# Kernel tuning notes

Hardware: AMD Instinct MI355X
Metric: run time of the kernel (lower is better)

The kernel has to match this reference:

```python
import jax, jax.numpy as jnp
import numpy as np

IN_CH = 128
HID = 256   # 2 * out_channels
OUT_CH = 128
N_NODES = 10000
N_EDGES = 640000


def setup_inputs() -> dict:
    key = jax.random.key(0)
    ks = jax.random.split(key, 6)
    x = jax.random.normal(ks[0], (N_NODES, IN_CH), dtype=jnp.float32)
    edge_index = jax.random.randint(ks[1], (2, N_EDGES), 0, N_NODES, dtype=jnp.int64)
    # GCNConv params (glorot-like scale)
    W1 = jax.random.normal(ks[2], (IN_CH, HID), dtype=jnp.float32) / np.sqrt(IN_CH)
    b1 = jnp.zeros((HID,), dtype=jnp.float32)
    W2 = jax.random.normal(ks[3], (HID, OUT_CH), dtype=jnp.float32) / np.sqrt(HID)
    b2 = jnp.zeros((OUT_CH,), dtype=jnp.float32)
    return {"x": x, "edge_index": edge_index, "W1": W1, "b1": b1, "W2": W2, "b2": b2}


def _gcn_norm(edge_index, n_nodes):
    """Add self-loops and compute symmetric GCN normalization per edge."""
    loops = jnp.arange(n_nodes, dtype=edge_index.dtype)
    src = jnp.concatenate([edge_index[0], loops])  # [E+N]
    dst = jnp.concatenate([edge_index[1], loops])
    deg = jax.ops.segment_sum(jnp.ones_like(dst, dtype=jnp.float32), dst,
                              num_segments=n_nodes)
    dinv = jnp.where(deg > 0, jax.lax.rsqrt(deg), 0.0)
    norm = dinv[src] * dinv[dst]  # [E+N]
    return src, dst, norm


def _gcn_layer(x, W, b, src, dst, norm, n_nodes):
    h = x @ W                                  # [N, F_out]
    msg = h[src] * norm[:, None]               # gather + scale, [E+N, F_out]
    agg = jax.ops.segment_sum(msg, dst, num_segments=n_nodes)
    return agg + b


def reference(x, edge_index, W1, b1, W2, b2):
    n = x.shape[0]
    src, dst, norm = _gcn_norm(edge_index, n)
    h = jax.nn.relu(_gcn_layer(x, W1, b1, src, dst, norm, n))
    out = jax.nn.relu(_gcn_layer(h, W2, b2, src, dst, norm, n))
    return out
```

## Files before the change

### kernel.cpp

```cpp
#include <hip/hip_runtime.h>

#define N_FEAT 128
#define HID 256
#define OUT_CH 128

#define NB 256
#define MAXN 10240
#define CH 16
#define CB (NB / CH)

__device__ __forceinline__ unsigned bf16rn(float f) {
    unsigned u = __float_as_uint(f);
    return (u + 0x7fffu + ((u >> 16) & 1u)) >> 16;
}
__device__ __forceinline__ unsigned pack_bf16x2(float lo, float hi) {
    return bf16rn(lo) | (bf16rn(hi) << 16);
}
__device__ __forceinline__ float2 unpack_bf16x2(unsigned u) {
    float2 r;
    r.x = __uint_as_float(u << 16);
    r.y = __uint_as_float(u & 0xffff0000u);
    return r;
}


__global__ __launch_bounds__(256)
void hist_kernel(const int* __restrict__ dst, unsigned short* __restrict__ bh,
                 int E, int N, int chunk) {
    __shared__ int hist[MAXN];
    for (int i = threadIdx.x; i < N; i += 256) hist[i] = 0;
    __syncthreads();
    int base = blockIdx.x * chunk;
    int lim = min(chunk, E - base);
    for (int i = threadIdx.x; i < lim; i += 256) {
        int d = dst[base + i];
        if (d >= 0 && d < N) atomicAdd(&hist[d], 1);
    }
    __syncthreads();
    unsigned short* out = bh + (size_t)blockIdx.x * N;
    for (int i = threadIdx.x; i < N; i += 256) out[i] = (unsigned short)hist[i];
}

__global__ __launch_bounds__(256)
void colsum_kernel(const unsigned short* __restrict__ bh,
                   int* __restrict__ ps, int N) {
    int j = blockIdx.x * 256 + threadIdx.x;
    if (j >= N) return;
    int c = blockIdx.y;
    int s = 0;
    #pragma unroll
    for (int b = c * CB; b < (c + 1) * CB; b++) s += bh[(size_t)b * N + j];
    ps[(size_t)c * N + j] = s;
}

__global__ __launch_bounds__(256)
void colscan_kernel(int* __restrict__ ps, int* __restrict__ counts, int N) {
    int j = blockIdx.x * 256 + threadIdx.x;
    if (j >= N) return;
    int run = 0;
    #pragma unroll
    for (int c = 0; c < CH; c++) {
        size_t idx = (size_t)c * N + j;
        int t = ps[idx];
        ps[idx] = run;
        run += t;
    }
    counts[j] = run;
}

#define SCAN_T 1024
#define SCAN_MAX_PER 16
__global__ __launch_bounds__(SCAN_T)
void scan_dinv_kernel(const int* __restrict__ counts,
                      int* __restrict__ row_start,
                      float* __restrict__ dinv, int n) {
    int tid = threadIdx.x;
    int per = (n + SCAN_T - 1) / SCAN_T;
    int base = tid * per;
    int local[SCAN_MAX_PER];
    int sum = 0;
    for (int j = 0; j < per; j++) {
        int i = base + j;
        int c = (i < n) ? counts[i] : 0;
        local[j] = sum;
        sum += c;
        if (i < n) dinv[i] = rsqrtf((float)(c + 1));
    }
    int lane = tid & 63;
    int wave = tid >> 6;
    int incl = sum;
    #pragma unroll
    for (int off = 1; off < 64; off <<= 1) {
        int t = __shfl_up(incl, off, 64);
        if (lane >= off) incl += t;
    }
    __shared__ int wsum[16];
    __shared__ int woff[16];
    if (lane == 63) wsum[wave] = incl;
    __syncthreads();
    if (wave == 0) {
        int w = (lane < 16) ? wsum[lane] : 0;
        int v = w;
        #pragma unroll
        for (int off = 1; off < 16; off <<= 1) {
            int t = __shfl_up(v, off, 64);
            if (lane >= off) v += t;
        }
        if (lane < 16) woff[lane] = v - w;
    }
    __syncthreads();
    int thread_excl = woff[wave] + (incl - sum);
    for (int j = 0; j < per; j++) {
        int i = base + j;
        if (i < n) row_start[i] = thread_excl + local[j];
    }
    if (tid == SCAN_T - 1) row_start[n] = thread_excl + sum;
}

__global__ __launch_bounds__(256)
void chunkbase_kernel(unsigned short* __restrict__ bh,
                      const int* __restrict__ ps, int N) {
    int j = blockIdx.x * 256 + threadIdx.x;
    if (j >= N) return;
    int c = blockIdx.y;
    int run = ps[(size_t)c * N + j];
    #pragma unroll
    for (int b = c * CB; b < (c + 1) * CB; b++) {
        size_t idx = (size_t)b * N + j;
        int t = bh[idx];
        bh[idx] = (unsigned short)run;
        run += t;
    }
}

__global__ __launch_bounds__(256)
void scat_kernel(const int* __restrict__ src, const int* __restrict__ dst,
                 const unsigned short* __restrict__ bh,
                 const int* __restrict__ row_start,
                 int* __restrict__ csr_src, int E, int N, int chunk) {
    __shared__ int cur[MAXN];
    const unsigned short* basep = bh + (size_t)blockIdx.x * N;
    for (int i = threadIdx.x; i < N; i += 256)
        cur[i] = row_start[i] + (int)basep[i];
    __syncthreads();
    int base = blockIdx.x * chunk;
    int lim = min(chunk, E - base);
    for (int i = threadIdx.x; i < lim; i += 256) {
        int e = base + i;
        int d = dst[e];
        if (d < 0 || d >= N) continue;
        int pos = atomicAdd(&cur[d], 1);
        if ((unsigned)pos < (unsigned)E) csr_src[pos] = src[e];
    }
}

__global__ void prescale_kernel(const float* __restrict__ x,
                                const float* __restrict__ dinv,
                                unsigned* __restrict__ xs_b, int total4) {
    int i = blockIdx.x * blockDim.x + threadIdx.x;
    if (i < total4) {
        int row = i >> 5;
        float d = dinv[row];
        float4 v = ((const float4*)x)[i];
        uint2 p;
        p.x = pack_bf16x2(v.x * d, v.y * d);
        p.y = pack_bf16x2(v.z * d, v.w * d);
        ((uint2*)xs_b)[i] = p;
    }
}

template <bool EPILOGUE>
__global__ __launch_bounds__(256)
void agg_kernel(const unsigned* __restrict__ featb,
                const float* __restrict__ dinv,
                const int* __restrict__ row_start,
                const int* __restrict__ csr_src,
                const float* __restrict__ bias,
                float* __restrict__ out, int N) {
    int wave = threadIdx.x >> 6;
    int n = blockIdx.x * 4 + wave;
    if (n >= N) return;
    int f = threadIdx.x & 63;
    float dn = dinv[n];
    float2 v = unpack_bf16x2(featb[(size_t)n * 64 + f]);
    float accx = v.x;
    float accy = v.y;
    int e0 = row_start[n];
    int e1 = row_start[n + 1];
    int e = e0;
    for (; e + 16 <= e1; e += 16) {
        int s[16];
        #pragma unroll
        for (int j = 0; j < 16; j++) s[j] = csr_src[e + j];
        unsigned w[16];
        #pragma unroll
        for (int j = 0; j < 16; j++) w[j] = featb[(size_t)s[j] * 64 + f];
        #pragma unroll
        for (int j = 0; j < 16; j++) {
            float2 u = unpack_bf16x2(w[j]);
            accx += u.x;
            accy += u.y;
        }
    }
    for (; e + 4 <= e1; e += 4) {
        int s0 = csr_src[e], s1 = csr_src[e + 1];
        int s2 = csr_src[e + 2], s3 = csr_src[e + 3];
        unsigned w0 = featb[(size_t)s0 * 64 + f];
        unsigned w1 = featb[(size_t)s1 * 64 + f];
        unsigned w2 = featb[(size_t)s2 * 64 + f];
        unsigned w3 = featb[(size_t)s3 * 64 + f];
        float2 u0 = unpack_bf16x2(w0), u1 = unpack_bf16x2(w1);
        float2 u2 = unpack_bf16x2(w2), u3 = unpack_bf16x2(w3);
        accx += u0.x + u1.x + u2.x + u3.x;
        accy += u0.y + u1.y + u2.y + u3.y;
    }
    for (; e < e1; ++e) {
        float2 u = unpack_bf16x2(featb[(size_t)csr_src[e] * 64 + f]);
        accx += u.x;
        accy += u.y;
    }
    accx *= dn;
    accy *= dn;
    if (EPILOGUE) {
        float2 b = ((const float2*)bias)[f];
        accx = fmaxf(accx + b.x, 0.0f);
        accy = fmaxf(accy + b.y, 0.0f);
    }
    float2 r;
    r.x = accx;
    r.y = accy;
    ((float2*)out)[(size_t)n * 64 + f] = r;
}

template <bool BIAS_RELU, bool RSCALE, bool BF16_OUT>
__global__ __launch_bounds__(256)
void gemm_kernel(const float* __restrict__ A,
                 const float* __restrict__ B,
                 const float* __restrict__ bias,
                 const float* __restrict__ rscale,
                 void* __restrict__ Cv, int M, int N, int K) {
    __shared__ float As[16][65];
    __shared__ float Bs[16][64];
    int tid = threadIdx.x;
    int n0 = blockIdx.x * 64;
    int m0 = blockIdx.y * 64;
    int tx = tid & 15;
    int ty = tid >> 4;
    float acc[4][4] = {};
    for (int k0 = 0; k0 < K; k0 += 16) {
        #pragma unroll
        for (int i = 0; i < 4; i++) {
            int lin = tid + 256 * i;
            int m = lin >> 4;
            int k = lin & 15;
            float v = 0.0f;
            if (m0 + m < M) v = A[(size_t)(m0 + m) * K + k0 + k];
            As[k][m] = v;
        }
        #pragma unroll
        for (int i = 0; i < 4; i++) {
            int lin = tid + 256 * i;
            int k = lin >> 6;
            int n = lin & 63;
            Bs[k][n] = B[(size_t)(k0 + k) * N + n0 + n];
        }
        __syncthreads();
        #pragma unroll
        for (int k = 0; k < 16; k++) {
            float ra[4], rb[4];
            #pragma unroll
            for (int i = 0; i < 4; i++) ra[i] = As[k][ty * 4 + i];
            #pragma unroll
            for (int j = 0; j < 4; j++) rb[j] = Bs[k][tx * 4 + j];
            #pragma unroll
            for (int i = 0; i < 4; i++)
                #pragma unroll
                for (int j = 0; j < 4; j++)
                    acc[i][j] = fmaf(ra[i], rb[j], acc[i][j]);
        }
        __syncthreads();
    }
    #pragma unroll
    for (int i = 0; i < 4; i++) {
        int m = m0 + ty * 4 + i;
        if (m >= M) continue;
        float rs = RSCALE ? rscale[m] : 1.0f;
        float v[4];
        #pragma unroll
        for (int j = 0; j < 4; j++) {
            v[j] = acc[i][j];
            if (RSCALE) v[j] *= rs;
            if (BIAS_RELU) v[j] = fmaxf(v[j] + bias[n0 + tx * 4 + j], 0.0f);
        }
        if (BF16_OUT) {
            unsigned* Cb = (unsigned*)Cv;
            size_t base = (size_t)m * (N >> 1) + ((n0 + tx * 4) >> 1);
            Cb[base] = pack_bf16x2(v[0], v[1]);
            Cb[base + 1] = pack_bf16x2(v[2], v[3]);
        } else {
            float* C = (float*)Cv;
            #pragma unroll
            for (int j = 0; j < 4; j++)
                C[(size_t)m * N + n0 + tx * 4 + j] = v[j];
        }
    }
}


static inline size_t align512(size_t x) { return (x + 511) & ~(size_t)511; }

extern "C" void kernel_launch(void* const* d_in, const int* in_sizes, int n_in,
                              void* d_out, int out_size, void* d_ws, size_t ws_size,
                              hipStream_t stream) {
    const float* x = (const float*)d_in[0];
    const int* ei = (const int*)d_in[1];
    const float* W1 = (const float*)d_in[2];
    const float* b1 = (const float*)d_in[3];
    const float* W2 = (const float*)d_in[4];
    const float* b2 = (const float*)d_in[5];
    float* out = (float*)d_out;

    const int N = in_sizes[0] / N_FEAT;
    const int E = in_sizes[1] / 2;
    const int* src = ei;
    const int* dst = ei + E;

    char* ws = (char*)d_ws;
    size_t off = 0;
    float* dinv = (float*)(ws + off);    off += align512((size_t)N * 4);
    int* counts = (int*)(ws + off);      off += align512((size_t)N * 4);
    int* row_start = (int*)(ws + off);   off += align512((size_t)(N + 1) * 4);
    int* csr_src = (int*)(ws + off);     off += align512((size_t)E * 4);
    unsigned* xs_b = (unsigned*)(ws + off); off += align512((size_t)N * 64 * 4);
    float* h = (float*)(ws + off);       off += align512((size_t)N * HID * 4);
    unsigned* t_b = (unsigned*)(ws + off); off += align512((size_t)N * 64 * 4);
    int* ps = (int*)(ws + off);          off += align512((size_t)CH * N * 4);
    unsigned short* bh = (unsigned short*)(ws + off);
    off += align512((size_t)NB * N * 2);
    (void)ws_size;
    float* agg1 = out;
    const int chunk = (E + NB - 1) / NB;
    const int NJ = (N + 255) / 256;

    hist_kernel<<<NB, 256, 0, stream>>>(dst, bh, E, N, chunk);
    colsum_kernel<<<dim3(NJ, CH), 256, 0, stream>>>(bh, ps, N);
    colscan_kernel<<<NJ, 256, 0, stream>>>(ps, counts, N);
    scan_dinv_kernel<<<1, SCAN_T, 0, stream>>>(counts, row_start, dinv, N);
    chunkbase_kernel<<<dim3(NJ, CH), 256, 0, stream>>>(bh, ps, N);
    scat_kernel<<<NB, 256, 0, stream>>>(src, dst, bh, row_start, csr_src, E, N, chunk);

    {
        int total4 = N * N_FEAT / 4;
        prescale_kernel<<<(total4 + 255) / 256, 256, 0, stream>>>(x, dinv, xs_b, total4);
    }

    agg_kernel<false><<<(N + 3) / 4, 256, 0, stream>>>(xs_b, dinv, row_start, csr_src,
                                                       nullptr, agg1, N);

    {
        dim3 grid(HID / 64, (N + 63) / 64);
        gemm_kernel<true, false, false><<<grid, 256, 0, stream>>>(
            agg1, W1, b1, nullptr, h, N, HID, N_FEAT);
    }

    {
        dim3 grid(OUT_CH / 64, (N + 63) / 64);
        gemm_kernel<false, true, true><<<grid, 256, 0, stream>>>(
            h, W2, nullptr, dinv, t_b, N, OUT_CH, HID);
    }

    agg_kernel<true><<<(N + 3) / 4, 256, 0, stream>>>(t_b, dinv, row_start, csr_src,
                                                      b2, out, N);
}
```

Baseline: 194.9 us.

## Split wave across two edges per step in aggregation, vectorize GEMM tile loads

The aggregation kernel now has each half-wave handle alternate edges, loading 8 bytes per lane and reading neighbour indices as int2 pairs. The two halves are combined with a cross-half shuffle. This gives wider gather transactions and more edges in flight per wave, at the cost of odd-start and odd-tail handling and idle lanes in those edge cases. The GEMM now stages A and B with float4 global loads and reads LDS as float4. The dinv computation moves from the single-block scan into the parallel colscan kernel, which shortens the serial scan.

After: 248.4 us. +27.4%, slower.

```diff
diff --git a/kernel.cpp b/kernel.cpp
--- a/kernel.cpp
+++ b/kernel.cpp
@@ -54,7 +54,8 @@
 }
 
 __global__ __launch_bounds__(256)
-void colscan_kernel(int* __restrict__ ps, int* __restrict__ counts, int N) {
+void colscan_kernel(int* __restrict__ ps, int* __restrict__ counts,
+                    float* __restrict__ dinv, int N) {
     int j = blockIdx.x * 256 + threadIdx.x;
     if (j >= N) return;
     int run = 0;
@@ -66,14 +67,14 @@
         run += t;
     }
     counts[j] = run;
+    dinv[j] = rsqrtf((float)(run + 1));
 }
 
 #define SCAN_T 1024
 #define SCAN_MAX_PER 16
 __global__ __launch_bounds__(SCAN_T)
-void scan_dinv_kernel(const int* __restrict__ counts,
-                      int* __restrict__ row_start,
-                      float* __restrict__ dinv, int n) {
+void scan_kernel(const int* __restrict__ counts,
+                 int* __restrict__ row_start, int n) {
     int tid = threadIdx.x;
     int per = (n + SCAN_T - 1) / SCAN_T;
     int base = tid * per;
@@ -84,7 +85,6 @@
         int c = (i < n) ? counts[i] : 0;
         local[j] = sum;
         sum += c;
-        if (i < n) dinv[i] = rsqrtf((float)(c + 1));
     }
     int lane = tid & 63;
     int wave = tid >> 6;
@@ -180,56 +180,73 @@
     int wave = threadIdx.x >> 6;
     int n = blockIdx.x * 4 + wave;
     if (n >= N) return;
-    int f = threadIdx.x & 63;
+    int l = threadIdx.x & 63;
+    int half = l >> 5;
+    int fl = l & 31;
+    const uint2* feat2 = (const uint2*)featb;
+    float a0 = 0.f, a1 = 0.f, a2 = 0.f, a3 = 0.f;
+    if (half == 0) {
+        uint2 s = feat2[(size_t)n * 32 + fl];
+        float2 u0 = unpack_bf16x2(s.x), u1 = unpack_bf16x2(s.y);
+        a0 = u0.x; a1 = u0.y; a2 = u1.x; a3 = u1.y;
+    }
+    int e0 = row_start[n], e1 = row_start[n + 1];
+    int e = e0;
+    if ((e & 1) && e < e1) {
+        if (half == 0) {
+            uint2 w = feat2[(size_t)csr_src[e] * 32 + fl];
+            float2 u0 = unpack_bf16x2(w.x), u1 = unpack_bf16x2(w.y);
+            a0 += u0.x; a1 += u0.y; a2 += u1.x; a3 += u1.y;
+        }
+        e++;
+    }
+    const int2* cs2 = (const int2*)csr_src;
+    for (; e + 32 <= e1; e += 32) {
+        int2 p[16];
+        #pragma unroll
+        for (int j = 0; j < 16; j++) p[j] = cs2[(e >> 1) + j];
+        uint2 w[16];
+        #pragma unroll
+        for (int j = 0; j < 16; j++) {
+            int s = half ? p[j].y : p[j].x;
+            w[j] = feat2[(size_t)s * 32 + fl];
+        }
+        #pragma unroll
+        for (int j = 0; j < 16; j++) {
+            float2 u0 = unpack_bf16x2(w[j].x), u1 = unpack_bf16x2(w[j].y);
+            a0 += u0.x; a1 += u0.y; a2 += u1.x; a3 += u1.y;
+        }
+    }
+    for (; e + 2 <= e1; e += 2) {
+        int2 p = cs2[e >> 1];
+        int s = half ? p.y : p.x;
+        uint2 w = feat2[(size_t)s * 32 + fl];
+        float2 u0 = unpack_bf16x2(w.x), u1 = unpack_bf16x2(w.y);
+        a0 += u0.x; a1 += u0.y; a2 += u1.x; a3 += u1.y;
+    }
+    if (e < e1 && half == 0) {
+        uint2 w = feat2[(size_t)csr_src[e] * 32 + fl];
+        float2 u0 = unpack_bf16x2(w.x), u1 = unpack_bf16x2(w.y);
+        a0 += u0.x; a1 += u0.y; a2 += u1.x; a3 += u1.y;
+    }
+    a0 += __shfl_xor(a0, 32, 64);
+    a1 += __shfl_xor(a1, 32, 64);
+    a2 += __shfl_xor(a2, 32, 64);
+    a3 += __shfl_xor(a3, 32, 64);
     float dn = dinv[n];
-    float2 v = unpack_bf16x2(featb[(size_t)n * 64 + f]);
-    float accx = v.x;
-    float accy = v.y;
-    int e0 = row_start[n];
-    int e1 = row_start[n + 1];
-    int e = e0;
-    for (; e + 16 <= e1; e += 16) {
-        int s[16];
-        #pragma unroll
-        for (int j = 0; j < 16; j++) s[j] = csr_src[e + j];
-        unsigned w[16];
-        #pragma unroll
-        for (int j = 0; j < 16; j++) w[j] = featb[(size_t)s[j] * 64 + f];
-        #pragma unroll
-        for (int j = 0; j < 16; j++) {
-            float2 u = unpack_bf16x2(w[j]);
-            accx += u.x;
-            accy += u.y;
-        }
-    }
-    for (; e + 4 <= e1; e += 4) {
-        int s0 = csr_src[e], s1 = csr_src[e + 1];
-        int s2 = csr_src[e + 2], s3 = csr_src[e + 3];
-        unsigned w0 = featb[(size_t)s0 * 64 + f];
-        unsigned w1 = featb[(size_t)s1 * 64 + f];
-        unsigned w2 = featb[(size_t)s2 * 64 + f];
-        unsigned w3 = featb[(size_t)s3 * 64 + f];
-        float2 u0 = unpack_bf16x2(w0), u1 = unpack_bf16x2(w1);
-        float2 u2 = unpack_bf16x2(w2), u3 = unpack_bf16x2(w3);
-        accx += u0.x + u1.x + u2.x + u3.x;
-        accy += u0.y + u1.y + u2.y + u3.y;
-    }
-    for (; e < e1; ++e) {
-        float2 u = unpack_bf16x2(featb[(size_t)csr_src[e] * 64 + f]);
-        accx += u.x;
-        accy += u.y;
-    }
-    accx *= dn;
-    accy *= dn;
+    a0 *= dn; a1 *= dn; a2 *= dn; a3 *= dn;
     if (EPILOGUE) {
-        float2 b = ((const float2*)bias)[f];
-        accx = fmaxf(accx + b.x, 0.0f);
-        accy = fmaxf(accy + b.y, 0.0f);
-    }
-    float2 r;
-    r.x = accx;
-    r.y = accy;
-    ((float2*)out)[(size_t)n * 64 + f] = r;
+        float4 b = ((const float4*)bias)[fl];
+        a0 = fmaxf(a0 + b.x, 0.0f);
+        a1 = fmaxf(a1 + b.y, 0.0f);
+        a2 = fmaxf(a2 + b.z, 0.0f);
+        a3 = fmaxf(a3 + b.w, 0.0f);
+    }
+    if (half == 0) {
+        float4 r;
+        r.x = a0; r.y = a1; r.z = a2; r.w = a3;
+        ((float4*)out)[(size_t)n * 32 + fl] = r;
+    }
 }
 
 template <bool BIAS_RELU, bool RSCALE, bool BF16_OUT>
@@ -239,44 +256,49 @@
                  const float* __restrict__ bias,
                  const float* __restrict__ rscale,
                  void* __restrict__ Cv, int M, int N, int K) {
-    __shared__ float As[16][65];
+    __shared__ float As[16][68];
     __shared__ float Bs[16][64];
     int tid = threadIdx.x;
     int n0 = blockIdx.x * 64;
     int m0 = blockIdx.y * 64;
     int tx = tid & 15;
     int ty = tid >> 4;
+    int ar = tid >> 2;
+    int akq = tid & 3;
+    int bk = tid >> 4;
+    int bnq = tid & 15;
     float acc[4][4] = {};
     for (int k0 = 0; k0 < K; k0 += 16) {
-        #pragma unroll
-        for (int i = 0; i < 4; i++) {
-            int lin = tid + 256 * i;
-            int m = lin >> 4;
-            int k = lin & 15;
-            float v = 0.0f;
-            if (m0 + m < M) v = A[(size_t)(m0 + m) * K + k0 + k];
-            As[k][m] = v;
-        }
-        #pragma unroll
-        for (int i = 0; i < 4; i++) {
-            int lin = tid + 256 * i;
-            int k = lin >> 6;
-            int n = lin & 63;
-            Bs[k][n] = B[(size_t)(k0 + k) * N + n0 + n];
-        }
+        float4 av = make_float4(0.f, 0.f, 0.f, 0.f);
+        if (m0 + ar < M)
+            av = *(const float4*)&A[(size_t)(m0 + ar) * K + k0 + akq * 4];
+        float4 bv = *(const float4*)&B[(size_t)(k0 + bk) * N + n0 + bnq * 4];
+        As[akq * 4 + 0][ar] = av.x;
+        As[akq * 4 + 1][ar] = av.y;
+        As[akq * 4 + 2][ar] = av.z;
+        As[akq * 4 + 3][ar] = av.w;
+        *(float4*)&Bs[bk][bnq * 4] = bv;
         __syncthreads();
         #pragma unroll
         for (int k = 0; k < 16; k++) {
-            float ra[4], rb[4];
-            #pragma unroll
-            for (int i = 0; i < 4; i++) ra[i] = As[k][ty * 4 + i];
-            #pragma unroll
-            for (int j = 0; j < 4; j++) rb[j] = Bs[k][tx * 4 + j];
-            #pragma unroll
-            for (int i = 0; i < 4; i++)
-                #pragma unroll
-                for (int j = 0; j < 4; j++)
-                    acc[i][j] = fmaf(ra[i], rb[j], acc[i][j]);
+            float4 ra = *(const float4*)&As[k][ty * 4];
+            float4 rb = *(const float4*)&Bs[k][tx * 4];
+            acc[0][0] = fmaf(ra.x, rb.x, acc[0][0]);
+            acc[0][1] = fmaf(ra.x, rb.y, acc[0][1]);
+            acc[0][2] = fmaf(ra.x, rb.z, acc[0][2]);
+            acc[0][3] = fmaf(ra.x, rb.w, acc[0][3]);
+            acc[1][0] = fmaf(ra.y, rb.x, acc[1][0]);
+            acc[1][1] = fmaf(ra.y, rb.y, acc[1][1]);
+            acc[1][2] = fmaf(ra.y, rb.z, acc[1][2]);
+            acc[1][3] = fmaf(ra.y, rb.w, acc[1][3]);
+            acc[2][0] = fmaf(ra.z, rb.x, acc[2][0]);
+            acc[2][1] = fmaf(ra.z, rb.y, acc[2][1]);
+            acc[2][2] = fmaf(ra.z, rb.z, acc[2][2]);
+            acc[2][3] = fmaf(ra.z, rb.w, acc[2][3]);
+            acc[3][0] = fmaf(ra.w, rb.x, acc[3][0]);
+            acc[3][1] = fmaf(ra.w, rb.y, acc[3][1]);
+            acc[3][2] = fmaf(ra.w, rb.z, acc[3][2]);
+            acc[3][3] = fmaf(ra.w, rb.w, acc[3][3]);
         }
         __syncthreads();
     }
@@ -344,8 +366,8 @@
 
     hist_kernel<<<NB, 256, 0, stream>>>(dst, bh, E, N, chunk);
     colsum_kernel<<<dim3(NJ, CH), 256, 0, stream>>>(bh, ps, N);
-    colscan_kernel<<<NJ, 256, 0, stream>>>(ps, counts, N);
-    scan_dinv_kernel<<<1, SCAN_T, 0, stream>>>(counts, row_start, dinv, N);
+    colscan_kernel<<<NJ, 256, 0, stream>>>(ps, counts, dinv, N);
+    scan_kernel<<<1, SCAN_T, 0, stream>>>(counts, row_start, N);
     chunkbase_kernel<<<dim3(NJ, CH), 256, 0, stream>>>(bh, ps, N);
     scat_kernel<<<NB, 256, 0, stream>>>(src, dst, bh, row_start, csr_src, E, N, chunk);
 
```
